# Kernel optimization log

Hardware: AMD Instinct MI355X
Metric: run time of the kernel (lower is better)

The kernel has to match this reference:

```python
import jax, jax.numpy as jnp
import numpy as np

# Multi-scale deformable attention encoder (Mask2Former pixel decoder transformer)
SHAPES = ((64, 64), (32, 32), (16, 16))  # (H, W) per level, strides 8/16/32 of 512x512
HEADS, POINTS, DM = 8, 4, 256
HD = DM // HEADS
NLVL = len(SHAPES)
NLAYERS = 6
STARTS = np.concatenate([[0], np.cumsum([h * w for h, w in SHAPES])])


def layer_norm(x, g, b, eps=1e-5):
    m = x.mean(-1, keepdims=True)
    v = ((x - m) ** 2).mean(-1, keepdims=True)
    return (x - m) * jax.lax.rsqrt(v + eps) * g + b


def ref_points(B, dtype):
    # valid_ratios == 1 (masks are all-False in the module)
    pts = []
    for H, W in SHAPES:
        ys = (jnp.arange(H, dtype=dtype) + 0.5) / H
        xs = (jnp.arange(W, dtype=dtype) + 0.5) / W
        gy, gx = jnp.meshgrid(ys, xs, indexing='ij')
        pts.append(jnp.stack([gx.reshape(-1), gy.reshape(-1)], -1))
    ref = jnp.concatenate(pts, 0)  # [Q,2]
    return jnp.broadcast_to(ref[None, :, None, :], (B, ref.shape[0], NLVL, 2))


def bilinear(value, loc, H, W):
    # grid_sample(align_corners=False, padding_mode='zeros')
    # value: [B,heads,H*W,d]; loc: [B,Q,heads,P,2] normalized to [0,1]
    x = loc[..., 0] * W - 0.5
    y = loc[..., 1] * H - 0.5
    x0f = jnp.floor(x); y0f = jnp.floor(y)
    lx = x - x0f; ly = y - y0f
    x0 = x0f.astype(jnp.int32); y0 = y0f.astype(jnp.int32)
    out = 0.
    for dx, dy, w in ((0, 0, (1 - lx) * (1 - ly)), (1, 0, lx * (1 - ly)),
                      (0, 1, (1 - lx) * ly), (1, 1, lx * ly)):
        xi = x0 + dx; yi = y0 + dy
        valid = (xi >= 0) & (xi < W) & (yi >= 0) & (yi < H)
        idx = jnp.clip(yi, 0, H - 1) * W + jnp.clip(xi, 0, W - 1)  # [B,Q,heads,P]
        idx_t = jnp.transpose(idx, (0, 2, 1, 3))  # [B,heads,Q,P]
        Bq, hq, Qq, Pq = idx_t.shape
        g = jnp.take_along_axis(value, idx_t.reshape(Bq, hq, Qq * Pq, 1), axis=2)
        g = g.reshape(Bq, hq, Qq, Pq, HD)
        wv = (w * valid).transpose(0, 2, 1, 3)[..., None]  # [B,heads,Q,P,1]
        out = out + g * wv
    return out  # [B,heads,Q,P,d]


def msda(query, src, ref, p):
    off_w, off_b, aw_w, aw_b, val_w, val_b, out_w, out_b = p
    B, Q, _ = query.shape
    value = (src @ val_w.T + val_b).reshape(B, Q, HEADS, HD).transpose(0, 2, 1, 3)  # [B,h,Q,d]
    off = (query @ off_w.T + off_b).reshape(B, Q, HEADS, NLVL, POINTS, 2)
    aw = (query @ aw_w.T + aw_b).reshape(B, Q, HEADS, NLVL * POINTS)
    aw = jax.nn.softmax(aw, -1).reshape(B, Q, HEADS, NLVL, POINTS)
    norm = jnp.array([[W, H] for H, W in SHAPES], dtype=query.dtype)  # [L,2] as (W,H)
    loc = ref[:, :, None, :, None, :] + off / norm[None, None, None, :, None, :]
    samp = []
    for l, (H, W) in enumerate(SHAPES):
        v = value[:, :, STARTS[l]:STARTS[l + 1], :]
        samp.append(bilinear(v, loc[:, :, :, l], H, W))  # [B,h,Q,P,d]
    samp = jnp.stack(samp, 3)  # [B,h,Q,L,P,d]
    w = aw.transpose(0, 2, 1, 3, 4)[..., None]  # [B,h,Q,L,P,1]
    o = (samp * w).sum((3, 4)).transpose(0, 2, 1, 3).reshape(B, Q, DM)
    return o @ out_w.T + out_b


def reference(src0, src1, src2, pos0, pos1, pos2, level_embed,
              off_w, off_b, aw_w, aw_b, val_w, val_b, out_w, out_b,
              ln1_g, ln1_b, ffn1_w, ffn1_b, ffn2_w, ffn2_b, ln2_g, ln2_b):
    srcs, poss = [src0, src1, src2], [pos0, pos1, pos2]
    B = src0.shape[0]
    xs, ps = [], []
    for l, (s, pe) in enumerate(zip(srcs, poss)):
        b, c, h, w = s.shape
        xs.append(s.reshape(b, c, h * w).transpose(0, 2, 1))
        ps.append(pe.reshape(b, c, h * w).transpose(0, 2, 1) + level_embed[l])
    x = jnp.concatenate(xs, 1)    # [B,Q,C]
    pos = jnp.concatenate(ps, 1)  # [B,Q,C]
    ref = ref_points(B, x.dtype)
    for i in range(NLAYERS):
        q = x + pos
        attn = msda(q, x, ref, (off_w[i], off_b[i], aw_w[i], aw_b[i],
                                val_w[i], val_b[i], out_w[i], out_b[i]))
        x = layer_norm(x + attn, ln1_g[i], ln1_b[i])
        h = jax.nn.relu(x @ ffn1_w[i].T + ffn1_b[i])
        x = layer_norm(x + h @ ffn2_w[i].T + ffn2_b[i], ln2_g[i], ln2_b[i])
    return x  # memory [B,Q,C]


def setup_inputs() -> dict:
    key = jax.random.key(0)
    ks = jax.random.split(key, 16)
    s = 0.02
    inp = {}
    inp['src0'] = jax.random.normal(ks[0], (4, 256, 64, 64), jnp.float32)
    inp['src1'] = jax.random.normal(ks[1], (4, 256, 32, 32), jnp.float32)
    inp['src2'] = jax.random.normal(ks[2], (4, 256, 16, 16), jnp.float32)
    inp['pos0'] = jax.random.normal(ks[3], (4, 256, 64, 64), jnp.float32)
    inp['pos1'] = jax.random.normal(ks[4], (4, 256, 32, 32), jnp.float32)
    inp['pos2'] = jax.random.normal(ks[5], (4, 256, 16, 16), jnp.float32)
    inp['level_embed'] = jax.random.normal(ks[6], (3, 256), jnp.float32)
    inp['off_w'] = jax.random.normal(ks[7], (6, 192, 256), jnp.float32) * s
    inp['off_b'] = jnp.zeros((6, 192), jnp.float32)
    inp['aw_w'] = jax.random.normal(ks[8], (6, 96, 256), jnp.float32) * s
    inp['aw_b'] = jnp.zeros((6, 96), jnp.float32)
    inp['val_w'] = jax.random.normal(ks[9], (6, 256, 256), jnp.float32) * s
    inp['val_b'] = jnp.zeros((6, 256), jnp.float32)
    inp['out_w'] = jax.random.normal(ks[10], (6, 256, 256), jnp.float32) * s
    inp['out_b'] = jnp.zeros((6, 256), jnp.float32)
    inp['ln1_g'] = jnp.ones((6, 256), jnp.float32)
    inp['ln1_b'] = jnp.zeros((6, 256), jnp.float32)
    inp['ffn1_w'] = jax.random.normal(ks[11], (6, 1024, 256), jnp.float32) * s
    inp['ffn1_b'] = jnp.zeros((6, 1024), jnp.float32)
    inp['ffn2_w'] = jax.random.normal(ks[12], (6, 256, 1024), jnp.float32) * s
    inp['ffn2_b'] = jnp.zeros((6, 256), jnp.float32)
    inp['ln2_g'] = jnp.ones((6, 256), jnp.float32)
    inp['ln2_b'] = jnp.zeros((6, 256), jnp.float32)
    return inp
```

## Files before the change

### kernel.cpp

```cpp
#include <hip/hip_runtime.h>
#include <hip/hip_bf16.h>
#include <math.h>

#define BB 4
#define QTOT 5376
#define DMM 256
#define NHEADS 8
#define HDIM 32
#define NPTS 4
#define NLVLS 3
#define BQ (BB*QTOT)
#define NOA 288

typedef short bf16x8 __attribute__((ext_vector_type(8)));
typedef unsigned short u16x8 __attribute__((ext_vector_type(8)));
typedef float f32x4  __attribute__((ext_vector_type(4)));

__device__ __forceinline__ unsigned short f2b(float f) {
  unsigned int u = __float_as_uint(f);
  unsigned int r = (u + 0x7FFFu + ((u >> 16) & 1u)) >> 16;
  return (unsigned short)r;
}
__device__ __forceinline__ float b2f(unsigned short u) {
  return __uint_as_float(((unsigned int)u) << 16);
}
__device__ __forceinline__ ushort4 f2b4(float4 v) {
  ushort4 o; o.x = f2b(v.x); o.y = f2b(v.y); o.z = f2b(v.z); o.w = f2b(v.w);
  return o;
}

__device__ __forceinline__ void gload16(const void* g, void* l) {
  __builtin_amdgcn_global_load_lds(
      (const __attribute__((address_space(1))) void*)g,
      (__attribute__((address_space(3))) void*)l, 16, 0, 0);
}

__global__ __launch_bounds__(256) void transpose_in(
    const float* __restrict__ src, const float* __restrict__ emb,
    float* __restrict__ dst, int HW, int qstart)
{
  __shared__ float t[32][33];
  int hw0 = blockIdx.x * 32, c0 = blockIdx.y * 32, b = blockIdx.z;
  int tx = threadIdx.x, ty = threadIdx.y;
  const float* s = src + ((size_t)b * DMM + c0) * HW + hw0;
#pragma unroll
  for (int j = 0; j < 4; j++)
    t[ty * 4 + j][tx] = s[(size_t)(ty * 4 + j) * HW + tx];
  __syncthreads();
  float e = emb ? emb[c0 + tx] : 0.0f;
  float* d = dst + ((size_t)b * QTOT + qstart + hw0) * DMM + c0;
#pragma unroll
  for (int j = 0; j < 4; j++)
    d[(size_t)(ty * 4 + j) * DMM + tx] = t[tx][ty * 4 + j] + e;
}

__global__ __launch_bounds__(256) void conv_b(
    const float* __restrict__ s, unsigned short* __restrict__ d, int n4)
{
  int i = blockIdx.x * 256 + threadIdx.x;
  if (i >= n4) return;
  ((ushort4*)d)[i] = f2b4(((const float4*)s)[i]);
}

__global__ __launch_bounds__(256) void pack_oa(
    const float* __restrict__ offw, const float* __restrict__ aww,
    unsigned short* __restrict__ dst)
{
  int i = blockIdx.x * 256 + threadIdx.x;
  if (i >= 6 * NOA * 64) return;
  int c4 = i & 63;
  int row = (i >> 6) % NOA;
  int l = i / (NOA * 64);
  const float* src = (row < 192)
      ? offw + ((size_t)l * 192 + row) * 256
      : aww  + ((size_t)l * 96 + (row - 192)) * 256;
  float4 v = ((const float4*)src)[c4];
  ((ushort4*)dst)[i] = f2b4(v);
}

__global__ __launch_bounds__(256) void pack_oa_bias(
    const float* __restrict__ offb, const float* __restrict__ awb,
    float* __restrict__ dst)
{
  int i = blockIdx.x * 256 + threadIdx.x;
  if (i >= 6 * NOA) return;
  int row = i % NOA, l = i / NOA;
  dst[i] = (row < 192) ? offb[l * 192 + row] : awb[l * 96 + (row - 192)];
}

__global__ __launch_bounds__(256) void prep(
    const float* __restrict__ x, const float* __restrict__ pos,
    unsigned short* __restrict__ xb, unsigned short* __restrict__ qb, int n4)
{
  int i = blockIdx.x * 256 + threadIdx.x;
  if (i >= n4) return;
  float4 a = ((const float4*)x)[i];
  float4 p = ((const float4*)pos)[i];
  ((ushort4*)xb)[i] = f2b4(a);
  float4 q = make_float4(a.x + p.x, a.y + p.y, a.z + p.z, a.w + p.w);
  ((ushort4*)qb)[i] = f2b4(q);
}


__device__ __forceinline__ void gemm_tile_body(
    const unsigned short* __restrict__ A, const unsigned short* __restrict__ W,
    int m0, int n0, int K,
    unsigned short (*As)[32], unsigned short (*Ws)[32], f32x4 acc[4][4])
{
  int tid = threadIdx.x;
  int wave = tid >> 6, lane = tid & 63;
  int lr = lane & 15;
  int lkr = ((lane >> 4) ^ (lane & 3)) * 8;
  int wrr = (wave >> 1) * 64;
  int wcc = (wave & 1) * 64;

  int srow = lane >> 2;
  int schunk = ((lane & 3) ^ (srow & 3)) * 8;
  const unsigned short* Ag = A + (size_t)(m0 + wave * 32 + srow) * K + schunk;
  const unsigned short* Wg = W + (size_t)(n0 + wave * 32 + srow) * K + schunk;

#define STAGE_BF(k0, buf)                                                      \
  { int bo = (buf) * 128 + wave * 32;                                          \
    gload16(Ag + (k0), &As[bo][0]);                                            \
    gload16(Ag + (size_t)16 * K + (k0), &As[bo + 16][0]);                      \
    gload16(Wg + (k0), &Ws[bo][0]);                                            \
    gload16(Wg + (size_t)16 * K + (k0), &Ws[bo + 16][0]); }

  STAGE_BF(0, 0);
  __syncthreads();
  int cur = 0;
  for (int k0 = 0; k0 < K; k0 += 32) {
    if (k0 + 32 < K) STAGE_BF(k0 + 32, cur ^ 1);
    int bo = cur * 128;
    bf16x8 af[4], bfv[4];
#pragma unroll
    for (int m = 0; m < 4; m++)
      af[m] = *(const bf16x8*)&As[bo + wrr + m * 16 + lr][lkr];
#pragma unroll
    for (int n = 0; n < 4; n++)
      bfv[n] = *(const bf16x8*)&Ws[bo + wcc + n * 16 + lr][lkr];
#pragma unroll
    for (int m = 0; m < 4; m++)
#pragma unroll
      for (int n = 0; n < 4; n++)
        acc[m][n] = __builtin_amdgcn_mfma_f32_16x16x32_bf16(af[m], bfv[n], acc[m][n], 0, 0, 0);
    __syncthreads();
    cur ^= 1;
  }
#undef STAGE_BF
}

__device__ __forceinline__ void gemm_epilogue(
    const float* __restrict__ bias, void* __restrict__ Cout,
    int m0, int n0, int N, int relu, int bfout, f32x4 acc[4][4])
{
  int tid = threadIdx.x;
  int wave = tid >> 6, lane = tid & 63;
  int lr = lane & 15;
  int wrr = (wave >> 1) * 64;
  int wcc = (wave & 1) * 64;
  float* C32 = (float*)Cout;
  unsigned short* C16 = (unsigned short*)Cout;
#pragma unroll
  for (int n = 0; n < 4; n++) {
    int col = n0 + wcc + n * 16 + lr;
    if (col >= N) continue;
    float bv = bias[col];
#pragma unroll
    for (int m = 0; m < 4; m++) {
      int row0 = m0 + wrr + m * 16 + (lane >> 4) * 4;
#pragma unroll
      for (int j = 0; j < 4; j++) {
        float v = acc[m][n][j] + bv;
        if (relu) v = fmaxf(v, 0.0f);
        if (bfout) C16[(size_t)(row0 + j) * N + col] = f2b(v);
        else       C32[(size_t)(row0 + j) * N + col] = v;
      }
    }
  }
}

__global__ __launch_bounds__(256) void gemm_bf(
    const unsigned short* __restrict__ A, const unsigned short* __restrict__ W,
    const float* __restrict__ bias, void* __restrict__ Cout,
    int M, int N, int K, int flags)
{
  __shared__ unsigned short As[256][32];
  __shared__ unsigned short Ws[256][32];
  f32x4 acc[4][4] = {};
  int m0 = blockIdx.x * 128, n0 = blockIdx.y * 128;
  gemm_tile_body(A, W, m0, n0, K, As, Ws, acc);
  gemm_epilogue(bias, Cout, m0, n0, N, flags & 1, flags & 2, acc);
}

__global__ __launch_bounds__(256) void gemm_valoa(
    const unsigned short* __restrict__ xb, const unsigned short* __restrict__ qb,
    const unsigned short* __restrict__ vW, const unsigned short* __restrict__ oaW,
    const float* __restrict__ vBias, const float* __restrict__ oaBias,
    unsigned short* __restrict__ valb16, float* __restrict__ offaw)
{
  __shared__ unsigned short As[256][32];
  __shared__ unsigned short Ws[256][32];
  f32x4 acc[4][4] = {};
  int m0 = blockIdx.x * 128;
  int by = blockIdx.y;
  const int K = 256;
  if (by < 2) {
    int n0 = by * 128;
    gemm_tile_body(xb, vW, m0, n0, K, As, Ws, acc);
    gemm_epilogue(vBias, valb16, m0, n0, 256, 0, 2, acc);
  } else {
    int n0 = (by - 2) * 128;
    gemm_tile_body(qb, oaW, m0, n0, K, As, Ws, acc);
    gemm_epilogue(oaBias, offaw, m0, n0, NOA, 0, 0, acc);
  }
}

__global__ __launch_bounds__(256) void gemm_ln(
    const unsigned short* __restrict__ A, const unsigned short* __restrict__ W,
    const float* __restrict__ bias, const float* __restrict__ g,
    const float* __restrict__ beta, float* __restrict__ x,
    unsigned short* __restrict__ xb, const float* __restrict__ pos,
    unsigned short* __restrict__ qb, int K)
{
  __shared__ unsigned short As[64][32];
  __shared__ unsigned short Ws[512][32];

  int m0 = blockIdx.x * 32;
  int tid = threadIdx.x;
  int wave = tid >> 6, lane = tid & 63;
  int lr = lane & 15;
  int lkr = ((lane >> 4) ^ (lane & 3)) * 8;
  int srow = lane >> 2;
  int schunk = ((lane & 3) ^ (srow & 3)) * 8;

  const unsigned short* Ag = A + (size_t)(m0 + (wave & 1) * 16 + srow) * K + schunk;
  const unsigned short* Wg = W + (size_t)(wave * 64 + srow) * K + schunk;

#define STAGE_LN(k0, buf)                                                      \
  { if (wave < 2) gload16(Ag + (k0), &As[(buf) * 32 + wave * 16][0]);          \
    gload16(Wg + (k0),                  &Ws[(buf) * 256 + wave * 64][0]);      \
    gload16(Wg + (size_t)16 * K + (k0), &Ws[(buf) * 256 + wave * 64 + 16][0]); \
    gload16(Wg + (size_t)32 * K + (k0), &Ws[(buf) * 256 + wave * 64 + 32][0]); \
    gload16(Wg + (size_t)48 * K + (k0), &Ws[(buf) * 256 + wave * 64 + 48][0]); }

  f32x4 acc[2][4] = {};

  STAGE_LN(0, 0);
  __syncthreads();
  int cur = 0;
  for (int k0 = 0; k0 < K; k0 += 32) {
    if (k0 + 32 < K) STAGE_LN(k0 + 32, cur ^ 1);
    bf16x8 af[2], bfv[4];
#pragma unroll
    for (int m = 0; m < 2; m++)
      af[m] = *(const bf16x8*)&As[cur * 32 + m * 16 + lr][lkr];
#pragma unroll
    for (int n = 0; n < 4; n++)
      bfv[n] = *(const bf16x8*)&Ws[cur * 256 + wave * 64 + n * 16 + lr][lkr];
#pragma unroll
    for (int m = 0; m < 2; m++)
#pragma unroll
      for (int n = 0; n < 4; n++)
        acc[m][n] = __builtin_amdgcn_mfma_f32_16x16x32_bf16(af[m], bfv[n], acc[m][n], 0, 0, 0);
    __syncthreads();
    cur ^= 1;
  }
#undef STAGE_LN

#pragma unroll
  for (int n = 0; n < 4; n++) {
    int col = wave * 64 + n * 16 + lr;
    float bv = bias[col];
#pragma unroll
    for (int m = 0; m < 2; m++) {
      int grow = m0 + m * 16 + (lane >> 4) * 4;
#pragma unroll
      for (int j = 0; j < 4; j++)
        acc[m][n][j] += bv + x[(size_t)(grow + j) * DMM + col];
    }
  }

  float2* red = (float2*)&As[0][0];
#pragma unroll
  for (int m = 0; m < 2; m++) {
#pragma unroll
    for (int j = 0; j < 4; j++) {
      float s  = acc[m][0][j] + acc[m][1][j] + acc[m][2][j] + acc[m][3][j];
      float s2 = acc[m][0][j] * acc[m][0][j] + acc[m][1][j] * acc[m][1][j]
               + acc[m][2][j] * acc[m][2][j] + acc[m][3][j] * acc[m][3][j];
#pragma unroll
      for (int o = 1; o < 16; o <<= 1) {
        s  += __shfl_xor(s,  o, 64);
        s2 += __shfl_xor(s2, o, 64);
      }
      if (lr == 0)
        red[(m * 16 + (lane >> 4) * 4 + j) * 4 + wave] = make_float2(s, s2);
    }
  }
  __syncthreads();

#pragma unroll
  for (int m = 0; m < 2; m++) {
    int rl0 = m * 16 + (lane >> 4) * 4;
#pragma unroll
    for (int j = 0; j < 4; j++) {
      int rl = rl0 + j;
      float2 r0 = red[rl * 4 + 0], r1 = red[rl * 4 + 1];
      float2 r2 = red[rl * 4 + 2], r3 = red[rl * 4 + 3];
      float ts  = r0.x + r1.x + r2.x + r3.x;
      float ts2 = r0.y + r1.y + r2.y + r3.y;
      float mean = ts * (1.0f / DMM);
      float var  = ts2 * (1.0f / DMM) - mean * mean;
      float sc = rsqrtf(var + 1e-5f);
      int grow = m0 + rl;
#pragma unroll
      for (int n = 0; n < 4; n++) {
        int col = wave * 64 + n * 16 + lr;
        float o = (acc[m][n][j] - mean) * sc * g[col] + beta[col];
        size_t idx = (size_t)grow * DMM + col;
        x[idx]  = o;
        xb[idx] = f2b(o);
        if (qb) qb[idx] = f2b(o + pos[idx]);
      }
    }
  }
}

__global__ __launch_bounds__(256) void msda_sample(
    const unsigned short* __restrict__ value, const float* __restrict__ offaw,
    unsigned short* __restrict__ attn16)
{
  __shared__ float soff[4][192];
  __shared__ float saw[4][96];
  __shared__ float smx[32], sinv[32];
  __shared__ float swgt[384 * 4];
  __shared__ int   sidx[384 * 4];

  int tid = threadIdx.x;
  int qi = tid >> 6, tq = tid & 63;
  int h = tq >> 3, dg = tq & 7;
  int bq0 = blockIdx.x * 4;
  int bq = bq0 + qi;
  int b = bq / QTOT;

  for (int i = tq; i < 192; i += 64) soff[qi][i] = offaw[(size_t)bq * NOA + i];
  for (int i = tq; i < 96;  i += 64) saw[qi][i]  = offaw[(size_t)bq * NOA + 192 + i];
  __syncthreads();

  if (tid < 32) {
    int q2 = tid >> 3, h2 = tid & 7;
    float mx = -1e30f;
#pragma unroll
    for (int t = 0; t < 12; t++) mx = fmaxf(mx, saw[q2][h2 * 12 + t]);
    float den = 0.f;
#pragma unroll
    for (int t = 0; t < 12; t++) den += __expf(saw[q2][h2 * 12 + t] - mx);
    smx[tid] = mx;
    sinv[tid] = 1.0f / den;
  }
  __syncthreads();

  for (int s = tid; s < 384; s += 256) {
    int p = s >> 5;
    int qh = s & 31;
    int q2 = qh >> 3, h2 = qh & 7;
    int l = p >> 2;
    int Wl = 64 >> l;
    int st = (l == 0) ? 0 : ((l == 1) ? 4096 : 5120);

    int q = (bq0 + q2) % QTOT;
    int qq, Wq;
    if (q < 4096)      { qq = q;        Wq = 64; }
    else if (q < 5120) { qq = q - 4096; Wq = 32; }
    else               { qq = q - 5120; Wq = 16; }
    float refx = ((qq % Wq) + 0.5f) / Wq;
    float refy = ((qq / Wq) + 0.5f) / Wq;

    int oi = ((h2 * NLVLS + l) * NPTS + (p & 3)) * 2;
    float invW = 1.0f / (float)Wl;
    float xf = (refx + soff[q2][oi]     * invW) * Wl - 0.5f;
    float yf = (refy + soff[q2][oi + 1] * invW) * Wl - 0.5f;
    float x0f = floorf(xf), y0f = floorf(yf);
    float fx = xf - x0f, fy = yf - y0f;
    int x0 = (int)x0f, y0 = (int)y0f;

    float aw = __expf(saw[q2][h2 * 12 + p] - smx[qh]) * sinv[qh];
    float w00 = (1.f - fx) * (1.f - fy) * aw;
    float w10 = fx * (1.f - fy) * aw;
    float w01 = (1.f - fx) * fy * aw;
    float w11 = fx * fy * aw;

    bool xv0 = (x0 >= 0) & (x0 < Wl);
    bool xv1 = (x0 + 1 >= 0) & (x0 + 1 < Wl);
    bool yv0 = (y0 >= 0) & (y0 < Wl);
    bool yv1 = (y0 + 1 >= 0) & (y0 + 1 < Wl);

    int base = s * 4;
    swgt[base + 0] = (xv0 & yv0) ? w00 : 0.f;
    swgt[base + 1] = (xv1 & yv0) ? w10 : 0.f;
    swgt[base + 2] = (xv0 & yv1) ? w01 : 0.f;
    swgt[base + 3] = (xv1 & yv1) ? w11 : 0.f;
    sidx[base + 0] = (xv0 & yv0) ? (st + y0 * Wl + x0) : 0;
    sidx[base + 1] = (xv1 & yv0) ? (st + y0 * Wl + x0 + 1) : 0;
    sidx[base + 2] = (xv0 & yv1) ? (st + (y0 + 1) * Wl + x0) : 0;
    sidx[base + 3] = (xv1 & yv1) ? (st + (y0 + 1) * Wl + x0 + 1) : 0;
  }
  __syncthreads();

  float4 acc = make_float4(0.f, 0.f, 0.f, 0.f);
  const unsigned short* vbase = value + (size_t)b * QTOT * DMM + h * HDIM + dg * 4;
#pragma unroll
  for (int p = 0; p < 12; p++) {
    int s3 = (p * 32 + qi * 8 + h) * 4;
    float4 w = *(const float4*)&swgt[s3];
    int4  ix = *(const int4*)&sidx[s3];
    ushort4 g0 = *(const ushort4*)(vbase + (size_t)ix.x * DMM);
    ushort4 g1 = *(const ushort4*)(vbase + (size_t)ix.y * DMM);
    ushort4 g2 = *(const ushort4*)(vbase + (size_t)ix.z * DMM);
    ushort4 g3 = *(const ushort4*)(vbase + (size_t)ix.w * DMM);
    acc.x += w.x * b2f(g0.x) + w.y * b2f(g1.x) + w.z * b2f(g2.x) + w.w * b2f(g3.x);
    acc.y += w.x * b2f(g0.y) + w.y * b2f(g1.y) + w.z * b2f(g2.y) + w.w * b2f(g3.y);
    acc.z += w.x * b2f(g0.z) + w.y * b2f(g1.z) + w.z * b2f(g2.z) + w.w * b2f(g3.z);
    acc.w += w.x * b2f(g0.w) + w.y * b2f(g1.w) + w.z * b2f(g2.w) + w.w * b2f(g3.w);
  }
  *(ushort4*)(attn16 + (size_t)bq * DMM + h * HDIM + dg * 4) = f2b4(acc);
}

extern "C" void kernel_launch(void* const* d_in, const int* in_sizes, int n_in,
                              void* d_out, int out_size, void* d_ws, size_t ws_size,
                              hipStream_t stream)
{
  const float* src[3] = {(const float*)d_in[0], (const float*)d_in[1], (const float*)d_in[2]};
  const float* pin[3] = {(const float*)d_in[3], (const float*)d_in[4], (const float*)d_in[5]};
  const float* lvl_emb = (const float*)d_in[6];
  const float* off_w = (const float*)d_in[7];
  const float* off_b = (const float*)d_in[8];
  const float* aw_w  = (const float*)d_in[9];
  const float* aw_b  = (const float*)d_in[10];
  const float* val_w = (const float*)d_in[11];
  const float* val_b = (const float*)d_in[12];
  const float* out_w = (const float*)d_in[13];
  const float* out_b = (const float*)d_in[14];
  const float* ln1_g = (const float*)d_in[15];
  const float* ln1_b = (const float*)d_in[16];
  const float* ffn1_w = (const float*)d_in[17];
  const float* ffn1_b = (const float*)d_in[18];
  const float* ffn2_w = (const float*)d_in[19];
  const float* ffn2_b = (const float*)d_in[20];
  const float* ln2_g = (const float*)d_in[21];
  const float* ln2_b = (const float*)d_in[22];

  float* x = (float*)d_out;

  char* wsp = (char*)d_ws;
  float* offaw = (float*)wsp;  wsp += (size_t)BQ * NOA * 4;
  unsigned short* valb16 = (unsigned short*)wsp; wsp += (size_t)BQ * 256 * 2;
  unsigned short* attnb  = (unsigned short*)wsp; wsp += (size_t)BQ * 256 * 2;
  unsigned short* hb = (unsigned short*)offaw;
  float* posb = (float*)wsp;  wsp += (size_t)BQ * 256 * 4;
  unsigned short* xb = (unsigned short*)wsp; wsp += (size_t)BQ * 256 * 2;
  unsigned short* qb = (unsigned short*)wsp; wsp += (size_t)BQ * 256 * 2;

  unsigned short* vWb  = (unsigned short*)wsp; wsp += (size_t)6 * 256 * 256 * 2;
  unsigned short* oaWb = (unsigned short*)wsp; wsp += (size_t)6 * NOA * 256 * 2;
  unsigned short* uWb  = (unsigned short*)wsp; wsp += (size_t)6 * 256 * 256 * 2;
  unsigned short* f1Wb = (unsigned short*)wsp; wsp += (size_t)6 * 1024 * 256 * 2;
  unsigned short* f2Wb = (unsigned short*)wsp; wsp += (size_t)6 * 256 * 1024 * 2;
  float* oaBias = (float*)wsp; wsp += (size_t)6 * NOA * 4;
  wsp += 65536;

  conv_b<<<(6 * 65536 / 4 + 255) / 256, 256, 0, stream>>>(val_w, vWb, 6 * 65536 / 4);
  conv_b<<<(6 * 65536 / 4 + 255) / 256, 256, 0, stream>>>(out_w, uWb, 6 * 65536 / 4);
  conv_b<<<(6 * 262144 / 4 + 255) / 256, 256, 0, stream>>>(ffn1_w, f1Wb, 6 * 262144 / 4);
  conv_b<<<(6 * 262144 / 4 + 255) / 256, 256, 0, stream>>>(ffn2_w, f2Wb, 6 * 262144 / 4);
  pack_oa<<<(6 * NOA * 64 + 255) / 256, 256, 0, stream>>>(off_w, aw_w, oaWb);
  pack_oa_bias<<<(6 * NOA + 255) / 256, 256, 0, stream>>>(off_b, aw_b, oaBias);

  const int HWs[3] = {4096, 1024, 256};
  const int starts[3] = {0, 4096, 5120};
  for (int l = 0; l < 3; l++) {
    dim3 g(HWs[l] / 32, DMM / 32, BB), blk(32, 8);
    transpose_in<<<g, blk, 0, stream>>>(src[l], nullptr, x, HWs[l], starts[l]);
    transpose_in<<<g, blk, 0, stream>>>(pin[l], lvl_emb + l * 256, posb, HWs[l], starts[l]);
  }
  prep<<<(BQ * 256 / 4 + 255) / 256, 256, 0, stream>>>(x, posb, xb, qb, BQ * 256 / 4);

  for (int i = 0; i < 6; i++) {
    gemm_valoa<<<dim3(BQ / 128, 5), 256, 0, stream>>>(
        xb, qb, vWb + (size_t)i * 65536, oaWb + (size_t)i * NOA * 256,
        val_b + i * 256, oaBias + i * NOA, valb16, offaw);
    msda_sample<<<BQ / 4, 256, 0, stream>>>(valb16, offaw, attnb);
    gemm_ln<<<BQ / 32, 256, 0, stream>>>(attnb, uWb + (size_t)i * 65536,
        out_b + i * 256, ln1_g + i * 256, ln1_b + i * 256, x, xb,
        nullptr, nullptr, 256);
    gemm_bf<<<dim3(BQ / 128, 8), 256, 0, stream>>>(xb, f1Wb + (size_t)i * 262144,
        ffn1_b + i * 1024, hb, BQ, 1024, 256, 1 | 2);
    gemm_ln<<<BQ / 32, 256, 0, stream>>>(hb, f2Wb + (size_t)i * 262144,
        ffn2_b + i * 256, ln2_g + i * 256, ln2_b + i * 256, x, xb,
        posb, qb, 1024);
  }
}
```

Before: 956.1 us.

## Process 8 queries per sampling block with 16-byte gathers and bf16 positional embedding

The deformable sampling kernel now handles 8 queries per block with 32 threads per query. Each thread gathers 8 bf16 channels (16 bytes) per corner instead of 4, and corner indices are precomputed as byte offsets. Offsets are read straight from global memory rather than staged in shared memory. Separately, the positional embedding is stored once as bf16, so the second LayerNorm GEMM reads half as many bytes when forming the next query; this adds a small extra rounding of pos.

```diff
diff --git a/kernel.cpp b/kernel.cpp
--- a/kernel.cpp
+++ b/kernel.cpp
@@ -90,17 +90,18 @@
 
 __global__ __launch_bounds__(256) void prep(
     const float* __restrict__ x, const float* __restrict__ pos,
-    unsigned short* __restrict__ xb, unsigned short* __restrict__ qb, int n4)
+    unsigned short* __restrict__ xb, unsigned short* __restrict__ qb,
+    unsigned short* __restrict__ pos16, int n4)
 {
   int i = blockIdx.x * 256 + threadIdx.x;
   if (i >= n4) return;
   float4 a = ((const float4*)x)[i];
   float4 p = ((const float4*)pos)[i];
   ((ushort4*)xb)[i] = f2b4(a);
+  ((ushort4*)pos16)[i] = f2b4(p);
   float4 q = make_float4(a.x + p.x, a.y + p.y, a.z + p.z, a.w + p.w);
   ((ushort4*)qb)[i] = f2b4(q);
 }
-
 
 __device__ __forceinline__ void gemm_tile_body(
     const unsigned short* __restrict__ A, const unsigned short* __restrict__ W,
@@ -220,7 +221,7 @@
     const unsigned short* __restrict__ A, const unsigned short* __restrict__ W,
     const float* __restrict__ bias, const float* __restrict__ g,
     const float* __restrict__ beta, float* __restrict__ x,
-    unsigned short* __restrict__ xb, const float* __restrict__ pos,
+    unsigned short* __restrict__ xb, const unsigned short* __restrict__ pos16,
     unsigned short* __restrict__ qb, int K)
 {
   __shared__ unsigned short As[64][32];
@@ -302,10 +303,9 @@
 
 #pragma unroll
   for (int m = 0; m < 2; m++) {
-    int rl0 = m * 16 + (lane >> 4) * 4;
 #pragma unroll
     for (int j = 0; j < 4; j++) {
-      int rl = rl0 + j;
+      int rl = m * 16 + (lane >> 4) * 4 + j;
       float2 r0 = red[rl * 4 + 0], r1 = red[rl * 4 + 1];
       float2 r2 = red[rl * 4 + 2], r3 = red[rl * 4 + 3];
       float ts  = r0.x + r1.x + r2.x + r3.x;
@@ -321,7 +321,7 @@
         size_t idx = (size_t)grow * DMM + col;
         x[idx]  = o;
         xb[idx] = f2b(o);
-        if (qb) qb[idx] = f2b(o + pos[idx]);
+        if (qb) qb[idx] = f2b(o + b2f(pos16[idx]));
       }
     }
   }
@@ -331,24 +331,23 @@
     const unsigned short* __restrict__ value, const float* __restrict__ offaw,
     unsigned short* __restrict__ attn16)
 {
-  __shared__ float soff[4][192];
-  __shared__ float saw[4][96];
-  __shared__ float smx[32], sinv[32];
-  __shared__ float swgt[384 * 4];
-  __shared__ int   sidx[384 * 4];
+  __shared__ float saw[8][96];
+  __shared__ float smx[64], sinv[64];
+  __shared__ float swgt[768 * 4];
+  __shared__ int   sofs[768 * 4];
 
   int tid = threadIdx.x;
-  int qi = tid >> 6, tq = tid & 63;
-  int h = tq >> 3, dg = tq & 7;
-  int bq0 = blockIdx.x * 4;
+  int qi = tid >> 5, t32 = tid & 31;
+  int h = t32 >> 2, dg = t32 & 3;
+  int bq0 = blockIdx.x * 8;
   int bq = bq0 + qi;
   int b = bq / QTOT;
 
-  for (int i = tq; i < 192; i += 64) soff[qi][i] = offaw[(size_t)bq * NOA + i];
-  for (int i = tq; i < 96;  i += 64) saw[qi][i]  = offaw[(size_t)bq * NOA + 192 + i];
-  __syncthreads();
-
-  if (tid < 32) {
+  for (int i = t32; i < 96; i += 32)
+    saw[qi][i] = offaw[(size_t)bq * NOA + 192 + i];
+  __syncthreads();
+
+  if (tid < 64) {
     int q2 = tid >> 3, h2 = tid & 7;
     float mx = -1e30f;
 #pragma unroll
@@ -361,9 +360,9 @@
   }
   __syncthreads();
 
-  for (int s = tid; s < 384; s += 256) {
-    int p = s >> 5;
-    int qh = s & 31;
+  for (int s = tid; s < 768; s += 256) {
+    int p = s >> 6;
+    int qh = s & 63;
     int q2 = qh >> 3, h2 = qh & 7;
     int l = p >> 2;
     int Wl = 64 >> l;
@@ -378,9 +377,10 @@
     float refy = ((qq / Wq) + 0.5f) / Wq;
 
     int oi = ((h2 * NLVLS + l) * NPTS + (p & 3)) * 2;
+    float2 off2 = *(const float2*)&offaw[(size_t)(bq0 + q2) * NOA + oi];
     float invW = 1.0f / (float)Wl;
-    float xf = (refx + soff[q2][oi]     * invW) * Wl - 0.5f;
-    float yf = (refy + soff[q2][oi + 1] * invW) * Wl - 0.5f;
+    float xf = (refx + off2.x * invW) * Wl - 0.5f;
+    float yf = (refy + off2.y * invW) * Wl - 0.5f;
     float x0f = floorf(xf), y0f = floorf(yf);
     float fx = xf - x0f, fy = yf - y0f;
     int x0 = (int)x0f, y0 = (int)y0f;
@@ -401,30 +401,35 @@
     swgt[base + 1] = (xv1 & yv0) ? w10 : 0.f;
     swgt[base + 2] = (xv0 & yv1) ? w01 : 0.f;
     swgt[base + 3] = (xv1 & yv1) ? w11 : 0.f;
-    sidx[base + 0] = (xv0 & yv0) ? (st + y0 * Wl + x0) : 0;
-    sidx[base + 1] = (xv1 & yv0) ? (st + y0 * Wl + x0 + 1) : 0;
-    sidx[base + 2] = (xv0 & yv1) ? (st + (y0 + 1) * Wl + x0) : 0;
-    sidx[base + 3] = (xv1 & yv1) ? (st + (y0 + 1) * Wl + x0 + 1) : 0;
-  }
-  __syncthreads();
-
-  float4 acc = make_float4(0.f, 0.f, 0.f, 0.f);
-  const unsigned short* vbase = value + (size_t)b * QTOT * DMM + h * HDIM + dg * 4;
+    sofs[base + 0] = (xv0 & yv0) ? (st + y0 * Wl + x0) * (DMM * 2) : 0;
+    sofs[base + 1] = (xv1 & yv0) ? (st + y0 * Wl + x0 + 1) * (DMM * 2) : 0;
+    sofs[base + 2] = (xv0 & yv1) ? (st + (y0 + 1) * Wl + x0) * (DMM * 2) : 0;
+    sofs[base + 3] = (xv1 & yv1) ? (st + (y0 + 1) * Wl + x0 + 1) * (DMM * 2) : 0;
+  }
+  __syncthreads();
+
+  float a8[8];
+#pragma unroll
+  for (int k = 0; k < 8; k++) a8[k] = 0.f;
+  const char* vbase = (const char*)(value + (size_t)b * QTOT * DMM + h * HDIM + dg * 8);
 #pragma unroll
   for (int p = 0; p < 12; p++) {
-    int s3 = (p * 32 + qi * 8 + h) * 4;
+    int s3 = (p * 64 + qi * 8 + h) * 4;
     float4 w = *(const float4*)&swgt[s3];
-    int4  ix = *(const int4*)&sidx[s3];
-    ushort4 g0 = *(const ushort4*)(vbase + (size_t)ix.x * DMM);
-    ushort4 g1 = *(const ushort4*)(vbase + (size_t)ix.y * DMM);
-    ushort4 g2 = *(const ushort4*)(vbase + (size_t)ix.z * DMM);
-    ushort4 g3 = *(const ushort4*)(vbase + (size_t)ix.w * DMM);
-    acc.x += w.x * b2f(g0.x) + w.y * b2f(g1.x) + w.z * b2f(g2.x) + w.w * b2f(g3.x);
-    acc.y += w.x * b2f(g0.y) + w.y * b2f(g1.y) + w.z * b2f(g2.y) + w.w * b2f(g3.y);
-    acc.z += w.x * b2f(g0.z) + w.y * b2f(g1.z) + w.z * b2f(g2.z) + w.w * b2f(g3.z);
-    acc.w += w.x * b2f(g0.w) + w.y * b2f(g1.w) + w.z * b2f(g2.w) + w.w * b2f(g3.w);
-  }
-  *(ushort4*)(attn16 + (size_t)bq * DMM + h * HDIM + dg * 4) = f2b4(acc);
+    int4  of = *(const int4*)&sofs[s3];
+    u16x8 g0 = *(const u16x8*)(vbase + of.x);
+    u16x8 g1 = *(const u16x8*)(vbase + of.y);
+    u16x8 g2 = *(const u16x8*)(vbase + of.z);
+    u16x8 g3 = *(const u16x8*)(vbase + of.w);
+#pragma unroll
+    for (int k = 0; k < 8; k++)
+      a8[k] += w.x * b2f((unsigned short)g0[k]) + w.y * b2f((unsigned short)g1[k])
+             + w.z * b2f((unsigned short)g2[k]) + w.w * b2f((unsigned short)g3[k]);
+  }
+  u16x8 o;
+#pragma unroll
+  for (int k = 0; k < 8; k++) o[k] = f2b(a8[k]);
+  *(u16x8*)(attn16 + (size_t)bq * DMM + h * HDIM + dg * 8) = o;
 }
 
 extern "C" void kernel_launch(void* const* d_in, const int* in_sizes, int n_in,
@@ -459,6 +464,7 @@
   unsigned short* attnb  = (unsigned short*)wsp; wsp += (size_t)BQ * 256 * 2;
   unsigned short* hb = (unsigned short*)offaw;
   float* posb = (float*)wsp;  wsp += (size_t)BQ * 256 * 4;
+  unsigned short* pos16 = (unsigned short*)wsp; wsp += (size_t)BQ * 256 * 2;
   unsigned short* xb = (unsigned short*)wsp; wsp += (size_t)BQ * 256 * 2;
   unsigned short* qb = (unsigned short*)wsp; wsp += (size_t)BQ * 256 * 2;
 
@@ -484,13 +490,13 @@
     transpose_in<<<g, blk, 0, stream>>>(src[l], nullptr, x, HWs[l], starts[l]);
     transpose_in<<<g, blk, 0, stream>>>(pin[l], lvl_emb + l * 256, posb, HWs[l], starts[l]);
   }
-  prep<<<(BQ * 256 / 4 + 255) / 256, 256, 0, stream>>>(x, posb, xb, qb, BQ * 256 / 4);
+  prep<<<(BQ * 256 / 4 + 255) / 256, 256, 0, stream>>>(x, posb, xb, qb, pos16, BQ * 256 / 4);
 
   for (int i = 0; i < 6; i++) {
     gemm_valoa<<<dim3(BQ / 128, 5), 256, 0, stream>>>(
         xb, qb, vWb + (size_t)i * 65536, oaWb + (size_t)i * NOA * 256,
         val_b + i * 256, oaBias + i * NOA, valb16, offaw);
-    msda_sample<<<BQ / 4, 256, 0, stream>>>(valb16, offaw, attnb);
+    msda_sample<<<BQ / 8, 256, 0, stream>>>(valb16, offaw, attnb);
     gemm_ln<<<BQ / 32, 256, 0, stream>>>(attnb, uWb + (size_t)i * 65536,
         out_b + i * 256, ln1_g + i * 256, ln1_b + i * 256, x, xb,
         nullptr, nullptr, 256);
@@ -498,6 +504,6 @@
         ffn1_b + i * 1024, hb, BQ, 1024, 256, 1 | 2);
     gemm_ln<<<BQ / 32, 256, 0, stream>>>(hb, f2Wb + (size_t)i * 262144,
         ffn2_b + i * 256, ln2_g + i * 256, ln2_b + i * 256, x, xb,
-        posb, qb, 1024);
-  }
-}
+        pos16, qb, 1024);
+  }
+}
```

Result: no change. 940.2 us (-1.7%).
